# Kernel optimization log

Hardware: AMD Instinct MI355X
Metric: run time of the kernel (lower is better)

The kernel has to match this reference:

```python
import jax, jax.numpy as jnp
import numpy as np

MIN_LEN = 4      # g.min_word_length
MAX_LEN = 10     # g.max_word_length
THRESH = 0.05    # g.init_threshold
NEG = -1e9


def setup_inputs() -> dict:
    key = jax.random.key(0)
    ks = jax.random.split(key, 6)
    B, L, F, D, U, V = 16, 64, 60, 256, 600, 10000
    x = jax.random.normal(ks[0], (B, L, F), jnp.float32)            # batch dense feat matrix
    unit_feats = jax.random.normal(ks[1], (U, F), jnp.float32)      # per-unit features
    W = jax.random.normal(ks[2], (F, D), jnp.float32) * 0.1         # FeatEmbedding weight
    lengths = jax.random.randint(ks[3], (B,), MIN_LEN, L + 1)       # sentence lengths
    indexed_segments = jax.random.randint(ks[4], (V, MAX_LEN), 0, U)  # vocab -> unit ids
    vocab_length = jax.random.randint(ks[5], (V,), MIN_LEN, MAX_LEN + 1)
    return dict(x=x, unit_feats=unit_feats, W=W, lengths=lengths,
                indexed_segments=indexed_segments, vocab_length=vocab_length)


def reference(x, unit_feats, W, lengths, indexed_segments, vocab_length):
    B, L, _ = x.shape
    V, J = indexed_segments.shape
    # embedding: features -> char_emb space
    word_repr = x @ W                 # [B, L, D]
    unit_repr = unit_feats @ W        # [U, D]
    # cosine similarity between every segment position and every unit
    wn = word_repr / (jnp.linalg.norm(word_repr, axis=-1, keepdims=True) + 1e-8)
    un = unit_repr / (jnp.linalg.norm(unit_repr, axis=-1, keepdims=True) + 1e-8)
    sim = jnp.einsum('bld,ud->blu', wn, un)  # [B, L, U]
    # pad so span gathers past the end read zeros (masked later by `viable`)
    sim_pad = jnp.pad(sim, ((0, 0), (0, J), (0, 0)))
    # accumulate per-position unit scores along each vocab word's unit sequence
    acc = jnp.zeros((B, L, V), sim.dtype)
    per_len = []
    for j in range(J):  # fixed small loop over word-length positions
        # sim at start+j for unit indexed_segments[v, j] -> [B, L, V]
        s_j = sim_pad[:, j:j + L, :][:, :, indexed_segments[:, j]]
        acc = acc + s_j
        if j + 1 >= MIN_LEN:
            per_len.append(acc / (j + 1))  # length-normalized match score
    scores = jnp.stack(per_len, axis=2)  # [B, len_s=L, len_e=E, V]
    E = scores.shape[2]
    k = jnp.arange(E) + MIN_LEN                          # candidate word lengths
    ends = jnp.arange(L)[:, None] + k[None, :] - 1        # [L, E]
    viable = ends[None] < lengths[:, None, None]          # [B, L, E]
    len_match = vocab_length[None, None, None, :] == k[None, None, :, None]
    mask = viable[..., None] & len_match                  # [B, L, E, V]
    masked = jnp.where(mask, scores, NEG)
    # best vocab word per span candidate
    value = masked.max(axis=-1)                           # [B, L, E]
    matched_vocab = masked.argmax(axis=-1)                # [B, L, E]
    matched = value > THRESH
    # best span candidate per batch element (eval path: hard max)
    flat = value.reshape(B, -1)                           # [B, L*E]
    best_inds = flat.argmax(axis=-1)
    best_scores = flat.max(axis=-1)
    best_starts = best_inds // E
    best_ends = best_inds % E + best_starts + MIN_LEN - 1
    any_matched = matched.reshape(B, -1).any(axis=-1)
    best_vocab = jnp.take_along_axis(matched_vocab.reshape(B, -1), best_inds[:, None], axis=1)[:, 0]
    return best_scores, best_starts, best_ends, any_matched, best_vocab
```

## Files before the change

kernel.cpp:

```cpp
#include <hip/hip_runtime.h>
#include <math.h>

#define BB 16
#define LL 64
#define FF 60
#define DD 256
#define UU 600
#define VV 10000
#define JMAX 10
#define MINL 4
#define EE 7
#define NEG (-1e9f)
#define TH 0.05f

#define UNT_OFF   0
#define UNT_SZ    (256 * 640)
#define WNT_OFF   (UNT_OFF + UNT_SZ)
#define WNT_SZ    (256 * 1024)
#define SIM_OFF   (WNT_OFF + WNT_SZ)
#define SIM_SZ    (BB * LL * UU)
#define PK_OFF    (SIM_OFF + SIM_SZ)
#define PK_SZ     (VV * 6)
#define VAL_OFF   (PK_OFF + PK_SZ)
#define VAL_SZ    (BB * LL * EE)
#define VOC_OFF   (VAL_OFF + VAL_SZ)

__global__ __launch_bounds__(256) void k_pack(const int* __restrict__ seg,
                                              const int* __restrict__ vlen,
                                              unsigned int* __restrict__ pk) {
    int v = blockIdx.x * 256 + threadIdx.x;
    if (v >= VV) return;
    const int* s = seg + v * JMAX;
    unsigned int t[10];
#pragma unroll
    for (int j = 0; j < JMAX; ++j) t[j] = (unsigned int)(s[j] * 11 + j);
    unsigned int* dst = pk + v * 6;
    dst[0] = t[0] | (t[1] << 16);
    dst[1] = t[2] | (t[3] << 16);
    dst[2] = t[4] | (t[5] << 16);
    dst[3] = t[6] | (t[7] << 16);
    dst[4] = t[8] | (t[9] << 16);
    dst[5] = (unsigned int)vlen[v];
}

__global__ __launch_bounds__(64) void k_embed(const float* __restrict__ x,
                                              const float* __restrict__ uf,
                                              const float* __restrict__ W,
                                              float* __restrict__ unT,
                                              float* __restrict__ wnT) {
    int id = blockIdx.x;
    int lane = threadIdx.x;
    const float* row;
    float* outB;
    int stride, col;
    if (id < UU) { row = uf + id * FF; outB = unT; stride = 640;  col = id; }
    else { int bl = id - UU; row = x + bl * FF; outB = wnT; stride = 1024; col = bl; }

    float r0 = 0.f, r1 = 0.f, r2 = 0.f, r3 = 0.f;
#pragma unroll 4
    for (int f = 0; f < FF; ++f) {
        float xv = row[f];
        r0 += xv * W[f * DD + lane];
        r1 += xv * W[f * DD + lane + 64];
        r2 += xv * W[f * DD + lane + 128];
        r3 += xv * W[f * DD + lane + 192];
    }
    float ss = r0 * r0 + r1 * r1 + r2 * r2 + r3 * r3;
#pragma unroll
    for (int m = 32; m > 0; m >>= 1) ss += __shfl_xor(ss, m, 64);
    float inv = 1.0f / (sqrtf(ss) + 1e-8f);
    outB[(lane      ) * stride + col] = r0 * inv;
    outB[(lane +  64) * stride + col] = r1 * inv;
    outB[(lane + 128) * stride + col] = r2 * inv;
    outB[(lane + 192) * stride + col] = r3 * inv;
}

__global__ __launch_bounds__(512, 2) void k_sim(const float* __restrict__ unT,
                                                const float* __restrict__ wnT,
                                                float* __restrict__ sim) {
    int blk = blockIdx.x;
    int b  = blk >> 4;
    int l0 = (blk & 15) * 4;
    int bl0 = b * 64 + l0;
    int tid = threadIdx.x;
    int w = tid >> 6;
    int lane = tid & 63;
    int u0 = w * 64 + lane;
    bool two = (w < 2);
    int u1 = two ? (512 + w * 64 + lane) : u0;

    float a00 = 0.f, a10 = 0.f, a20 = 0.f, a30 = 0.f;
    float a01 = 0.f, a11 = 0.f, a21 = 0.f, a31 = 0.f;

#pragma unroll 4
    for (int d = 0; d < DD; ++d) {
        float w0 = wnT[d * 1024 + bl0 + 0];
        float w1 = wnT[d * 1024 + bl0 + 1];
        float w2 = wnT[d * 1024 + bl0 + 2];
        float w3 = wnT[d * 1024 + bl0 + 3];
        float v0 = unT[d * 640 + u0];
        float v1 = unT[d * 640 + u1];
        a00 += w0 * v0; a01 += w0 * v1;
        a10 += w1 * v0; a11 += w1 * v1;
        a20 += w2 * v0; a21 += w2 * v1;
        a30 += w3 * v0; a31 += w3 * v1;
    }
    sim[(bl0 + 0) * UU + u0] = a00;
    sim[(bl0 + 1) * UU + u0] = a10;
    sim[(bl0 + 2) * UU + u0] = a20;
    sim[(bl0 + 3) * UU + u0] = a30;
    if (two && u1 < UU) {
        sim[(bl0 + 0) * UU + u1] = a01;
        sim[(bl0 + 1) * UU + u1] = a11;
        sim[(bl0 + 2) * UU + u1] = a21;
        sim[(bl0 + 3) * UU + u1] = a31;
    }
}

__global__ __launch_bounds__(512, 4) void k_score(const float* __restrict__ sim,
                                                  const unsigned int* __restrict__ pk,
                                                  const int* __restrict__ lengths,
                                                  float* __restrict__ val,
                                                  int* __restrict__ voc) {
    __shared__ float lds[UU * 11];
    __shared__ float redS[14][8];
    __shared__ int   redV[14][8];

    int blk = blockIdx.x;
    int b  = blk >> 5;
    int l0 = (blk & 31) * 2;
    int tid = threadIdx.x;

    for (int u = tid; u < UU; u += 512) {
#pragma unroll
        for (int r = 0; r < 11; ++r) {
            int m = l0 + r;
            lds[u * 11 + r] = (m < LL) ? sim[(b * 64 + m) * UU + u] : 0.0f;
        }
    }
    __syncthreads();

    float bS[EE][2];
    int   bV[EE][2];
#pragma unroll
    for (int e = 0; e < EE; ++e) {
        bS[e][0] = -1e30f; bS[e][1] = -1e30f;
        bV[e][0] = 0;      bV[e][1] = 0;
    }

    for (int v = tid; v < VV; v += 512) {
        const uint2* pp = (const uint2*)(pk + v * 6);
        uint2 q0 = pp[0];
        uint2 q1 = pp[1];
        uint2 q2 = pp[2];
        int idx[10];
        idx[0] = q0.x & 0xffff; idx[1] = q0.x >> 16;
        idx[2] = q0.y & 0xffff; idx[3] = q0.y >> 16;
        idx[4] = q1.x & 0xffff; idx[5] = q1.x >> 16;
        idx[6] = q1.y & 0xffff; idx[7] = q1.y >> 16;
        idx[8] = q2.x & 0xffff; idx[9] = q2.x >> 16;
        int k = (int)(q2.y & 0xffff);

        float a0 = 0.f, a1 = 0.f;
#pragma unroll
        for (int j = 0; j < JMAX; ++j) {
            float x0 = lds[idx[j]];
            float x1 = lds[idx[j] + 1];
            a0 += x0;
            a1 += x1;
            if (j >= MINL - 1) {
                int e = j - (MINL - 1);
                bool m = (k == j + 1);
                bool p0 = m & (a0 > bS[e][0]);
                bool p1 = m & (a1 > bS[e][1]);
                bS[e][0] = p0 ? a0 : bS[e][0];
                bV[e][0] = p0 ? v  : bV[e][0];
                bS[e][1] = p1 ? a1 : bS[e][1];
                bV[e][1] = p1 ? v  : bV[e][1];
            }
        }
    }

    int w = tid >> 6, lane = tid & 63;
#pragma unroll
    for (int e = 0; e < EE; ++e) {
#pragma unroll
        for (int dl = 0; dl < 2; ++dl) {
            float s = bS[e][dl];
            int vv = bV[e][dl];
#pragma unroll
            for (int off = 32; off > 0; off >>= 1) {
                float os = __shfl_down(s, off, 64);
                int   ov = __shfl_down(vv, off, 64);
                if (os > s || (os == s && ov < vv)) { s = os; vv = ov; }
            }
            if (lane == 0) { redS[e * 2 + dl][w] = s; redV[e * 2 + dl][w] = vv; }
        }
    }
    __syncthreads();

    if (tid < 14) {
        int e  = tid >> 1;
        int dl = tid & 1;
        float s = redS[tid][0];
        int  vv = redV[tid][0];
#pragma unroll
        for (int w2 = 1; w2 < 8; ++w2) {
            float os = redS[tid][w2];
            int   ov = redV[tid][w2];
            if (os > s || (os == s && ov < vv)) { s = os; vv = ov; }
        }
        int lg = l0 + dl;
        int k = e + MINL;
        bool viable = (lg + k - 1) < lengths[b];
        float sn = s / (float)k;
        val[(b * 64 + lg) * EE + e] = viable ? sn : NEG;
        voc[(b * 64 + lg) * EE + e] = viable ? vv : 0;
    }
}

__global__ __launch_bounds__(512) void k_final(const float* __restrict__ val,
                                               const int* __restrict__ voc,
                                               float* __restrict__ out) {
    __shared__ float sS[8];
    __shared__ int   sI[8];
    __shared__ int   sA[8];
    int b = blockIdx.x;
    int t = threadIdx.x;
    float s = -3e38f;
    int idx = 1 << 30;
    int any = 0;
    if (t < LL * EE) {
        s = val[b * LL * EE + t];
        idx = t;
        any = (s > TH) ? 1 : 0;
    }
#pragma unroll
    for (int off = 32; off > 0; off >>= 1) {
        float os = __shfl_down(s, off, 64);
        int   oi = __shfl_down(idx, off, 64);
        int   oa = __shfl_down(any, off, 64);
        if (os > s || (os == s && oi < idx)) { s = os; idx = oi; }
        any |= oa;
    }
    int w = t >> 6, lane = t & 63;
    if (lane == 0) { sS[w] = s; sI[w] = idx; sA[w] = any; }
    __syncthreads();
    if (t == 0) {
        for (int w2 = 1; w2 < 8; ++w2) {
            float os = sS[w2];
            int   oi = sI[w2];
            if (os > s || (os == s && oi < idx)) { s = os; idx = oi; }
            any |= sA[w2];
        }
        int start = idx / EE;
        int e = idx - start * EE;
        int end = e + start + MINL - 1;
        int vocab = voc[b * LL * EE + idx];
        out[b]      = s;
        out[16 + b] = (float)start;
        out[32 + b] = (float)end;
        out[48 + b] = any ? 1.0f : 0.0f;
        out[64 + b] = (float)vocab;
    }
}

extern "C" void kernel_launch(void* const* d_in, const int* in_sizes, int n_in,
                              void* d_out, int out_size, void* d_ws, size_t ws_size,
                              hipStream_t stream) {
    const float* x       = (const float*)d_in[0];
    const float* uf      = (const float*)d_in[1];
    const float* W       = (const float*)d_in[2];
    const int*   lengths = (const int*)d_in[3];
    const int*   seg     = (const int*)d_in[4];
    const int*   vlen    = (const int*)d_in[5];
    float* out = (float*)d_out;
    float* ws  = (float*)d_ws;

    float*        unT = ws + UNT_OFF;
    float*        wnT = ws + WNT_OFF;
    float*        sim = ws + SIM_OFF;
    unsigned int* pk  = (unsigned int*)(ws + PK_OFF);
    float*        val = ws + VAL_OFF;
    int*          voc = (int*)(ws + VOC_OFF);

    k_pack<<<(VV + 255) / 256, 256, 0, stream>>>(seg, vlen, pk);
    k_embed<<<UU + BB * LL, 64, 0, stream>>>(x, uf, W, unT, wnT);
    k_sim<<<256, 512, 0, stream>>>(unT, wnT, sim);
    k_score<<<512, 512, 0, stream>>>(sim, pk, lengths, val, voc);
    k_final<<<BB, 512, 0, stream>>>(val, voc, out);
}
```

Before: 146.9 us.

## Split vocab scan across two block halves and shrink sim tiles for more parallelism

The scoring kernel now splits the vocabulary into two halves handled by separate blocks, doubling the grid to 1024 blocks. The final kernel merges the two partial results per span. The similarity kernel uses smaller tiles (2 rows by 320 units) across 1024 blocks, and packed vocab entries are padded to 32 bytes so they load as two uint4 reads. This aims to fill more CUs on the GPU, at the cost of loading the sim rows into LDS twice and doing less register reuse per block in k_sim.

After: 147.8 us. About the same (+0.6%).

```diff
diff --git a/kernel.cpp b/kernel.cpp
--- a/kernel.cpp
+++ b/kernel.cpp
@@ -12,6 +12,7 @@
 #define EE 7
 #define NEG (-1e9f)
 #define TH 0.05f
+#define VHALF (VV / 2)
 
 #define UNT_OFF   0
 #define UNT_SZ    (256 * 640)
@@ -20,9 +21,9 @@
 #define SIM_OFF   (WNT_OFF + WNT_SZ)
 #define SIM_SZ    (BB * LL * UU)
 #define PK_OFF    (SIM_OFF + SIM_SZ)
-#define PK_SZ     (VV * 6)
+#define PK_SZ     (VV * 8)
 #define VAL_OFF   (PK_OFF + PK_SZ)
-#define VAL_SZ    (BB * LL * EE)
+#define VAL_SZ    (2 * BB * LL * EE)
 #define VOC_OFF   (VAL_OFF + VAL_SZ)
 
 __global__ __launch_bounds__(256) void k_pack(const int* __restrict__ seg,
@@ -34,13 +35,15 @@
     unsigned int t[10];
 #pragma unroll
     for (int j = 0; j < JMAX; ++j) t[j] = (unsigned int)(s[j] * 11 + j);
-    unsigned int* dst = pk + v * 6;
+    unsigned int* dst = pk + v * 8;
     dst[0] = t[0] | (t[1] << 16);
     dst[1] = t[2] | (t[3] << 16);
     dst[2] = t[4] | (t[5] << 16);
     dst[3] = t[6] | (t[7] << 16);
     dst[4] = t[8] | (t[9] << 16);
     dst[5] = (unsigned int)vlen[v];
+    dst[6] = 0;
+    dst[7] = 0;
 }
 
 __global__ __launch_bounds__(64) void k_embed(const float* __restrict__ x,
@@ -75,49 +78,36 @@
     outB[(lane + 192) * stride + col] = r3 * inv;
 }
 
-__global__ __launch_bounds__(512, 2) void k_sim(const float* __restrict__ unT,
+__global__ __launch_bounds__(320, 5) void k_sim(const float* __restrict__ unT,
                                                 const float* __restrict__ wnT,
                                                 float* __restrict__ sim) {
     int blk = blockIdx.x;
-    int b  = blk >> 4;
-    int l0 = (blk & 15) * 4;
+    int b  = blk >> 6;
+    int r  = blk & 63;
+    int l0 = (r >> 1) * 2;
+    int uh = r & 1;
     int bl0 = b * 64 + l0;
     int tid = threadIdx.x;
     int w = tid >> 6;
     int lane = tid & 63;
-    int u0 = w * 64 + lane;
-    bool two = (w < 2);
-    int u1 = two ? (512 + w * 64 + lane) : u0;
-
-    float a00 = 0.f, a10 = 0.f, a20 = 0.f, a30 = 0.f;
-    float a01 = 0.f, a11 = 0.f, a21 = 0.f, a31 = 0.f;
-
-#pragma unroll 4
+    int u = uh * 320 + w * 64 + lane;
+
+    float a0 = 0.f, a1 = 0.f;
+#pragma unroll 8
     for (int d = 0; d < DD; ++d) {
         float w0 = wnT[d * 1024 + bl0 + 0];
         float w1 = wnT[d * 1024 + bl0 + 1];
-        float w2 = wnT[d * 1024 + bl0 + 2];
-        float w3 = wnT[d * 1024 + bl0 + 3];
-        float v0 = unT[d * 640 + u0];
-        float v1 = unT[d * 640 + u1];
-        a00 += w0 * v0; a01 += w0 * v1;
-        a10 += w1 * v0; a11 += w1 * v1;
-        a20 += w2 * v0; a21 += w2 * v1;
-        a30 += w3 * v0; a31 += w3 * v1;
-    }
-    sim[(bl0 + 0) * UU + u0] = a00;
-    sim[(bl0 + 1) * UU + u0] = a10;
-    sim[(bl0 + 2) * UU + u0] = a20;
-    sim[(bl0 + 3) * UU + u0] = a30;
-    if (two && u1 < UU) {
-        sim[(bl0 + 0) * UU + u1] = a01;
-        sim[(bl0 + 1) * UU + u1] = a11;
-        sim[(bl0 + 2) * UU + u1] = a21;
-        sim[(bl0 + 3) * UU + u1] = a31;
-    }
-}
-
-__global__ __launch_bounds__(512, 4) void k_score(const float* __restrict__ sim,
+        float v  = unT[d * 640 + u];
+        a0 += w0 * v;
+        a1 += w1 * v;
+    }
+    if (u < UU) {
+        sim[(bl0 + 0) * UU + u] = a0;
+        sim[(bl0 + 1) * UU + u] = a1;
+    }
+}
+
+__global__ __launch_bounds__(512, 8) void k_score(const float* __restrict__ sim,
                                                   const unsigned int* __restrict__ pk,
                                                   const int* __restrict__ lengths,
                                                   float* __restrict__ val,
@@ -127,8 +117,10 @@
     __shared__ int   redV[14][8];
 
     int blk = blockIdx.x;
-    int b  = blk >> 5;
-    int l0 = (blk & 31) * 2;
+    int half = blk >> 9;
+    int rest = blk & 511;
+    int b  = rest >> 5;
+    int l0 = (rest & 31) * 2;
     int tid = threadIdx.x;
 
     for (int u = tid; u < UU; u += 512) {
@@ -148,18 +140,18 @@
         bV[e][0] = 0;      bV[e][1] = 0;
     }
 
-    for (int v = tid; v < VV; v += 512) {
-        const uint2* pp = (const uint2*)(pk + v * 6);
-        uint2 q0 = pp[0];
-        uint2 q1 = pp[1];
-        uint2 q2 = pp[2];
+    int vend = VHALF * (half + 1);
+    for (int v = VHALF * half + tid; v < vend; v += 512) {
+        const uint4* pp = (const uint4*)(pk + v * 8);
+        uint4 qa = pp[0];
+        uint4 qb = pp[1];
         int idx[10];
-        idx[0] = q0.x & 0xffff; idx[1] = q0.x >> 16;
-        idx[2] = q0.y & 0xffff; idx[3] = q0.y >> 16;
-        idx[4] = q1.x & 0xffff; idx[5] = q1.x >> 16;
-        idx[6] = q1.y & 0xffff; idx[7] = q1.y >> 16;
-        idx[8] = q2.x & 0xffff; idx[9] = q2.x >> 16;
-        int k = (int)(q2.y & 0xffff);
+        idx[0] = qa.x & 0xffff; idx[1] = qa.x >> 16;
+        idx[2] = qa.y & 0xffff; idx[3] = qa.y >> 16;
+        idx[4] = qa.z & 0xffff; idx[5] = qa.z >> 16;
+        idx[6] = qa.w & 0xffff; idx[7] = qa.w >> 16;
+        idx[8] = qb.x & 0xffff; idx[9] = qb.x >> 16;
+        int k = (int)(qb.y & 0xffff);
 
         float a0 = 0.f, a1 = 0.f;
 #pragma unroll
@@ -214,8 +206,9 @@
         int k = e + MINL;
         bool viable = (lg + k - 1) < lengths[b];
         float sn = s / (float)k;
-        val[(b * 64 + lg) * EE + e] = viable ? sn : NEG;
-        voc[(b * 64 + lg) * EE + e] = viable ? vv : 0;
+        int o = (half * BB * LL + b * 64 + lg) * EE + e;
+        val[o] = viable ? sn : NEG;
+        voc[o] = viable ? vv : 0;
     }
 }
 
@@ -224,14 +217,21 @@
                                                float* __restrict__ out) {
     __shared__ float sS[8];
     __shared__ int   sI[8];
+    __shared__ int   sV[8];
     __shared__ int   sA[8];
     int b = blockIdx.x;
     int t = threadIdx.x;
     float s = -3e38f;
     int idx = 1 << 30;
+    int vc = 0;
     int any = 0;
     if (t < LL * EE) {
-        s = val[b * LL * EE + t];
+        int o0 = b * LL * EE + t;
+        int o1 = BB * LL * EE + o0;
+        float s0 = val[o0], s1 = val[o1];
+        bool sel = s1 > s0;
+        s  = sel ? s1 : s0;
+        vc = sel ? voc[o1] : voc[o0];
         idx = t;
         any = (s > TH) ? 1 : 0;
     }
@@ -239,29 +239,29 @@
     for (int off = 32; off > 0; off >>= 1) {
         float os = __shfl_down(s, off, 64);
         int   oi = __shfl_down(idx, off, 64);
+        int   ov = __shfl_down(vc, off, 64);
         int   oa = __shfl_down(any, off, 64);
-        if (os > s || (os == s && oi < idx)) { s = os; idx = oi; }
+        if (os > s || (os == s && oi < idx)) { s = os; idx = oi; vc = ov; }
         any |= oa;
     }
     int w = t >> 6, lane = t & 63;
-    if (lane == 0) { sS[w] = s; sI[w] = idx; sA[w] = any; }
+    if (lane == 0) { sS[w] = s; sI[w] = idx; sV[w] = vc; sA[w] = any; }
     __syncthreads();
     if (t == 0) {
         for (int w2 = 1; w2 < 8; ++w2) {
             float os = sS[w2];
             int   oi = sI[w2];
-            if (os > s || (os == s && oi < idx)) { s = os; idx = oi; }
+            if (os > s || (os == s && oi < idx)) { s = os; idx = oi; vc = sV[w2]; }
             any |= sA[w2];
         }
         int start = idx / EE;
         int e = idx - start * EE;
         int end = e + start + MINL - 1;
-        int vocab = voc[b * LL * EE + idx];
         out[b]      = s;
         out[16 + b] = (float)start;
         out[32 + b] = (float)end;
         out[48 + b] = any ? 1.0f : 0.0f;
-        out[64 + b] = (float)vocab;
+        out[64 + b] = (float)vc;
     }
 }
 
@@ -286,7 +286,7 @@
 
     k_pack<<<(VV + 255) / 256, 256, 0, stream>>>(seg, vlen, pk);
     k_embed<<<UU + BB * LL, 64, 0, stream>>>(x, uf, W, unT, wnT);
-    k_sim<<<256, 512, 0, stream>>>(unT, wnT, sim);
-    k_score<<<512, 512, 0, stream>>>(sim, pk, lengths, val, voc);
+    k_sim<<<1024, 320, 0, stream>>>(unT, wnT, sim);
+    k_score<<<1024, 512, 0, stream>>>(sim, pk, lengths, val, voc);
     k_final<<<BB, 512, 0, stream>>>(val, voc, out);
 }
```
